# Kernel optimization log

Measured on AMD Instinct MI355X. Metric: run time of the kernel, lower is better.

## Reference

```python
import jax, jax.numpy as jnp
import numpy as np

N, E = 40000, 640000
IN_DIM, HID, HEADS, OUT, NC, ASSIGN = 128, 16, 8, 128, 2, 100
SIGMA = 0.5
F_HID = HID * HEADS  # 128 = hidden_dim * n_heads


def _edge_softmax(logits, dst, n):
    # softmax over incoming edges of each destination node (DGL edge_softmax)
    m = jax.ops.segment_max(logits, dst, num_segments=n)
    ex = jnp.exp(logits - m[dst])
    den = jax.ops.segment_sum(ex, dst, num_segments=n)
    return ex / den[dst]


def _gat_conv(h, src, dst, W, al, ar, b):
    # DGL GATConv: fc (no bias) -> per-head additive attention -> edge softmax -> scatter-sum
    nH, D = al.shape
    feat = (h @ W).reshape(h.shape[0], nH, D)            # [N,H,D]
    el = (feat * al).sum(-1)                              # [N,H]
    er = (feat * ar).sum(-1)                              # [N,H]
    logits = jax.nn.leaky_relu(el[src] + er[dst], 0.2)    # [E,H]
    a = _edge_softmax(logits, dst, h.shape[0])            # [E,H]
    out = jax.ops.segment_sum(feat[src] * a[..., None], dst, num_segments=h.shape[0])
    return out + b                                        # [N,H,D]


def _bn(x, g, b, eps=1e-5):
    mu = x.mean(0)
    v = x.var(0)
    return g * (x - mu) * jax.lax.rsqrt(v + eps) + b


def _gat_layer(h, src, dst, W, al, ar, b, g, bt):
    x = _gat_conv(h, src, dst, W, al, ar, b).reshape(h.shape[0], -1)
    x = jax.nn.elu(_bn(x, g, bt))
    return h + x  # residual: in_dim == out_dim*heads


def _mask(x):
    # h[torch.isinf(h)] = 1e9
    return jnp.where(jnp.isinf(x), 1e9, x)


def setup_inputs():
    key = jax.random.key(0)
    ks = jax.random.split(key, 20)
    rn = lambda k, s: jax.random.normal(k, s, jnp.float32) * 0.1
    return {
        "h": jax.random.normal(ks[0], (N, IN_DIM), jnp.float32),
        "e": jax.random.normal(ks[1], (E, 4), jnp.float32),
        "src": jax.random.randint(ks[2], (E,), 0, N, jnp.int32),
        "dst": jax.random.randint(ks[3], (E,), 0, N, jnp.int32),
        "W_emb": rn(ks[4], (IN_DIM, F_HID)), "b_emb": jnp.zeros((F_HID,), jnp.float32),
        "Wg": rn(ks[5], (3, F_HID, F_HID)),
        "alg": rn(ks[6], (3, HEADS, HID)), "arg": rn(ks[7], (3, HEADS, HID)),
        "bg": jnp.zeros((3, HEADS, HID), jnp.float32),
        "gam": jnp.ones((3, F_HID), jnp.float32), "bet": jnp.zeros((3, F_HID), jnp.float32),
        "W3": rn(ks[8], (F_HID, OUT)), "al3": rn(ks[9], (1, OUT)), "ar3": rn(ks[10], (1, OUT)),
        "b3": jnp.zeros((1, OUT), jnp.float32),
        "gam3": jnp.ones((OUT,), jnp.float32), "bet3": jnp.zeros((OUT,), jnp.float32),
        "Wa": rn(ks[11], (F_HID, ASSIGN)), "ba": jnp.zeros((ASSIGN,), jnp.float32),
        "Wm1": rn(ks[12], (2 * OUT, OUT)), "bm1": jnp.zeros((OUT,), jnp.float32),
        "Wm2": rn(ks[13], (OUT, OUT // 2)), "bm2": jnp.zeros((OUT // 2,), jnp.float32),
        "Wm3": rn(ks[14], (OUT // 2, NC)), "bm3": jnp.zeros((NC,), jnp.float32),
    }


def reference(h, e, src, dst, W_emb, b_emb, Wg, alg, arg, bg, gam, bet,
              W3, al3, ar3, b3, gam3, bet3, Wa, ba,
              Wm1, bm1, Wm2, bm2, Wm3, bm3):
    del e  # edge_feat=False: forward never consumes edge features
    h = h @ W_emb + b_emb  # embedding_h (dropout p=0 -> identity)
    # layer 0: GATLayer
    h = _mask(_gat_layer(h, src, dst, Wg[0], alg[0], arg[0], bg[0], gam[0], bet[0]))
    # layer 1: biGATLayer -> (h, s): GAT update + soft assignment s with sigma mixing over coarse pool
    h_in = h
    h_fine = _gat_layer(h, src, dst, Wg[1], alg[1], arg[1], bg[1], gam[1], bet[1])
    s = jax.nn.softmax(h_in @ Wa + ba, axis=-1)            # [N, ASSIGN]
    h_coarse = s.T @ h_fine                                # [ASSIGN, F_HID]
    h = _mask(SIGMA * h_fine + (1.0 - SIGMA) * (s @ h_coarse))
    # layer 2: GATLayer
    h = _mask(_gat_layer(h, src, dst, Wg[2], alg[2], arg[2], bg[2], gam[2], bet[2]))
    # layer 3: GATLayer, 1 head, out_dim
    h = _mask(_gat_layer(h, src, dst, W3, al3, ar3, b3, gam3, bet3))
    # apply_edges: gather src/dst node feats, concat, MLPReadout (256->128->64->NC), inf-mask
    z = jnp.concatenate([h[src], h[dst]], axis=1)          # [E, 2*OUT]
    z = jax.nn.relu(z @ Wm1 + bm1)
    z = jax.nn.relu(z @ Wm2 + bm2)
    z = _mask(z @ Wm3 + bm3)
    return z, s
```

## Files before the change

### kernel.cpp

```cpp
#include <hip/hip_runtime.h>
#include <hip/hip_bf16.h>
#include <math.h>

#define N_ 40000
#define E_ 640000
#define CB_ 400
#define CR_ 100
#define SB_ 256
#define SNB_ 157

typedef short bf16x8 __attribute__((ext_vector_type(8)));
typedef float floatx4 __attribute__((ext_vector_type(4)));

__device__ __forceinline__ short f2bf(float f) {
    __hip_bfloat16 h = __float2bfloat16(f);
    return *reinterpret_cast<short*>(&h);
}
__device__ __forceinline__ float bf2f(short u) {
    unsigned int x = ((unsigned int)(unsigned short)u) << 16;
    return __int_as_float(x);
}
__device__ __forceinline__ float rdlane(float v, int l) {
    return __int_as_float(__builtin_amdgcn_readlane(__float_as_int(v), l));
}
__device__ __forceinline__ float bflo(unsigned int u) { return __int_as_float(u << 16); }
__device__ __forceinline__ float bfhi(unsigned int u) { return __int_as_float(u & 0xffff0000u); }

__global__ void k_count(const int* __restrict__ dst, int* __restrict__ counts) {
    for (int e = blockIdx.x * blockDim.x + threadIdx.x; e < E_; e += gridDim.x * blockDim.x)
        atomicAdd(&counts[dst[e]], 1);
}

__global__ __launch_bounds__(256) void k_scanA(const int* __restrict__ counts,
                                               int* __restrict__ excl,
                                               int* __restrict__ bsum) {
    int t = threadIdx.x;
    int i = blockIdx.x * SB_ + t;
    int v = (i < N_) ? counts[i] : 0;
    int lane = t & 63, wv = t >> 6;
    int x = v;
#pragma unroll
    for (int off = 1; off < 64; off <<= 1) {
        int y = __shfl_up(x, off);
        if (lane >= off) x += y;
    }
    __shared__ int wsum[4];
    __shared__ int woff[4];
    if (lane == 63) wsum[wv] = x;
    __syncthreads();
    if (t == 0) {
        int a = 0;
#pragma unroll
        for (int j = 0; j < 4; j++) { int tv = wsum[j]; woff[j] = a; a += tv; }
        bsum[blockIdx.x] = a;
    }
    __syncthreads();
    if (i < N_) excl[i] = x - v + woff[wv];
}

__global__ __launch_bounds__(256) void k_scanB(int* __restrict__ bsum) {
    int t = threadIdx.x;
    int v = (t < SNB_) ? bsum[t] : 0;
    int lane = t & 63, wv = t >> 6;
    int x = v;
#pragma unroll
    for (int off = 1; off < 64; off <<= 1) {
        int y = __shfl_up(x, off);
        if (lane >= off) x += y;
    }
    __shared__ int wsum[4];
    __shared__ int woff[4];
    if (lane == 63) wsum[wv] = x;
    __syncthreads();
    if (t == 0) {
        int a = 0;
#pragma unroll
        for (int j = 0; j < 4; j++) { int tv = wsum[j]; woff[j] = a; a += tv; }
    }
    __syncthreads();
    if (t < SNB_) bsum[t] = x - v + woff[wv];
}

__global__ __launch_bounds__(256) void k_scanC(const int* __restrict__ excl,
                                               const int* __restrict__ bsum,
                                               int* __restrict__ rowptr,
                                               int* __restrict__ cursor) {
    int i = blockIdx.x * 256 + threadIdx.x;
    if (i < N_) {
        int r = excl[i] + bsum[i / SB_];
        rowptr[i] = r;
        cursor[i] = r;
    }
    if (i == N_) rowptr[N_] = E_;
}

__global__ void k_fill(const int* __restrict__ src, const int* __restrict__ dst,
                       int* __restrict__ cursor, int* __restrict__ srcv,
                       unsigned short* __restrict__ dstv, int* __restrict__ eidv) {
    for (int e = blockIdx.x * blockDim.x + threadIdx.x; e < E_; e += gridDim.x * blockDim.x) {
        int d = dst[e];
        int pos = atomicAdd(&cursor[d], 1);
        srcv[pos] = src[e];
        dstv[pos] = (unsigned short)d;
        eidv[pos] = e;
    }
}

__global__ __launch_bounds__(256) void k_prep_all(const float* __restrict__ Wg,
                                                  const float* __restrict__ W3,
                                                  const float* __restrict__ Wm1,
                                                  short* __restrict__ WbT6) {
    int i = blockIdx.x * 256 + threadIdx.x;
    if (i >= 6 * 16384) return;
    int m = i >> 14;
    int r = i & 16383;
    int n = r >> 7, k = r & 127;
    const float* srcp;
    switch (m) {
        case 0: srcp = Wg; break;
        case 1: srcp = Wg + 16384; break;
        case 2: srcp = Wg + 32768; break;
        case 3: srcp = W3; break;
        case 4: srcp = Wm1; break;
        default: srcp = Wm1 + 16384; break;
    }
    WbT6[m * 16384 + n * 128 + k] = f2bf(srcp[k * 128 + n]);
}

__global__ __launch_bounds__(256) void k_prep_hilo(const float* __restrict__ W_emb,
                                                   const float* __restrict__ Wa,
                                                   short* __restrict__ WembT_hi,
                                                   short* __restrict__ WembT_lo,
                                                   short* __restrict__ WaT_hi,
                                                   short* __restrict__ WaT_lo) {
    int i = blockIdx.x * 256 + threadIdx.x;
    if (i >= 2 * 16384) return;
    int m = i >> 14;
    int r = i & 16383;
    int n = r >> 7, k = r & 127;
    if (m == 0) {
        float w = W_emb[k * 128 + n];
        short h = f2bf(w);
        WembT_hi[n * 128 + k] = h;
        WembT_lo[n * 128 + k] = f2bf(w - bf2f(h));
    } else {
        float w = (n < 100) ? Wa[k * 100 + n] : 0.f;
        short h = f2bf(w);
        WaT_hi[n * 128 + k] = h;
        WaT_lo[n * 128 + k] = f2bf(w - bf2f(h));
    }
}

__global__ __launch_bounds__(256) void k_mfma_hilo(const float* __restrict__ A,
                                                   const short* __restrict__ BT_hi,
                                                   const short* __restrict__ BT_lo,
                                                   const float* __restrict__ bias,
                                                   float* __restrict__ C, int ncols) {
    __shared__ short sAh[64 * 136];
    __shared__ short sAl[64 * 136];
    __shared__ short sBh[128 * 136];
    int t = threadIdx.x;
    int r0 = blockIdx.x * 64;
    {
        int n = t >> 1;
        int k0 = (t & 1) * 64;
#pragma unroll
        for (int j = 0; j < 8; j++) {
            bf16x8 v = *(const bf16x8*)(BT_hi + n * 128 + k0 + 8 * j);
            *(bf16x8*)(sBh + n * 136 + k0 + 8 * j) = v;
        }
    }
    {
        int r = t >> 2;
        int k0 = (t & 3) * 32;
        const float* ar = A + (size_t)(r0 + r) * 128 + k0;
#pragma unroll
        for (int j = 0; j < 4; j++) {
            float4 f0 = *(const float4*)(ar + 8 * j);
            float4 f1 = *(const float4*)(ar + 8 * j + 4);
            float x[8] = {f0.x, f0.y, f0.z, f0.w, f1.x, f1.y, f1.z, f1.w};
            bf16x8 vh, vl;
#pragma unroll
            for (int q = 0; q < 8; q++) {
                short hh = f2bf(x[q]);
                vh[q] = hh;
                vl[q] = f2bf(x[q] - bf2f(hh));
            }
            *(bf16x8*)(sAh + r * 136 + k0 + 8 * j) = vh;
            *(bf16x8*)(sAl + r * 136 + k0 + 8 * j) = vl;
        }
    }
    __syncthreads();
    int lane = t & 63, wv = t >> 6;
    int lm = lane & 15, quad = lane >> 4;
    int m0 = wv * 16;
    bf16x8 aH[4], aL[4];
#pragma unroll
    for (int kt = 0; kt < 4; kt++) {
        aH[kt] = *(const bf16x8*)(sAh + (m0 + lm) * 136 + kt * 32 + quad * 8);
        aL[kt] = *(const bf16x8*)(sAl + (m0 + lm) * 136 + kt * 32 + quad * 8);
    }
#pragma unroll
    for (int nt = 0; nt < 8; nt++) {
        const short* blp = BT_lo + (nt * 16 + lm) * 128 + quad * 8;
        floatx4 acc = (floatx4){0.f, 0.f, 0.f, 0.f};
#pragma unroll
        for (int kt = 0; kt < 4; kt++) {
            bf16x8 bH = *(const bf16x8*)(sBh + (nt * 16 + lm) * 136 + kt * 32 + quad * 8);
            bf16x8 bL = *(const bf16x8*)(blp + kt * 32);
            acc = __builtin_amdgcn_mfma_f32_16x16x32_bf16(aH[kt], bH, acc, 0, 0, 0);
            acc = __builtin_amdgcn_mfma_f32_16x16x32_bf16(aL[kt], bH, acc, 0, 0, 0);
            acc = __builtin_amdgcn_mfma_f32_16x16x32_bf16(aH[kt], bL, acc, 0, 0, 0);
        }
        int col = nt * 16 + lm;
        if (col < ncols) {
            float bv = bias ? bias[col] : 0.f;
#pragma unroll
            for (int r = 0; r < 4; r++) {
                int row = r0 + m0 + quad * 4 + r;
                C[(size_t)row * ncols + col] = acc[r] + bv;
            }
        }
    }
}

__global__ __launch_bounds__(256) void k_gemm_mfma(const float* __restrict__ A,
                                                   const short* __restrict__ WbT,
                                                   const float* __restrict__ bias,
                                                   short* __restrict__ C) {
    __shared__ short sA[64 * 136];
    __shared__ short sB[128 * 136];
    int t = threadIdx.x;
    int r0 = blockIdx.x * 64;
    {
        int n = t >> 1;
        int k0 = (t & 1) * 64;
#pragma unroll
        for (int j = 0; j < 8; j++) {
            bf16x8 v = *(const bf16x8*)(WbT + n * 128 + k0 + 8 * j);
            *(bf16x8*)(sB + n * 136 + k0 + 8 * j) = v;
        }
    }
    {
        int r = t >> 2;
        int k0 = (t & 3) * 32;
        const float* ar = A + (size_t)(r0 + r) * 128 + k0;
#pragma unroll
        for (int j = 0; j < 4; j++) {
            float4 f0 = *(const float4*)(ar + 8 * j);
            float4 f1 = *(const float4*)(ar + 8 * j + 4);
            bf16x8 v;
            v[0] = f2bf(f0.x); v[1] = f2bf(f0.y); v[2] = f2bf(f0.z); v[3] = f2bf(f0.w);
            v[4] = f2bf(f1.x); v[5] = f2bf(f1.y); v[6] = f2bf(f1.z); v[7] = f2bf(f1.w);
            *(bf16x8*)(sA + r * 136 + k0 + 8 * j) = v;
        }
    }
    __syncthreads();
    int lane = t & 63, wv = t >> 6;
    int lm = lane & 15, quad = lane >> 4;
    int m0 = wv * 16;
    bf16x8 aF[4];
#pragma unroll
    for (int kt = 0; kt < 4; kt++)
        aF[kt] = *(const bf16x8*)(sA + (m0 + lm) * 136 + kt * 32 + quad * 8);
#pragma unroll
    for (int nt = 0; nt < 8; nt++) {
        floatx4 acc = (floatx4){0.f, 0.f, 0.f, 0.f};
#pragma unroll
        for (int kt = 0; kt < 4; kt++) {
            bf16x8 bF = *(const bf16x8*)(sB + (nt * 16 + lm) * 136 + kt * 32 + quad * 8);
            acc = __builtin_amdgcn_mfma_f32_16x16x32_bf16(aF[kt], bF, acc, 0, 0, 0);
        }
        int col = nt * 16 + lm;
        float bv = bias ? bias[col] : 0.f;
#pragma unroll
        for (int r = 0; r < 4; r++) {
            int row = r0 + m0 + quad * 4 + r;
            C[(size_t)row * 128 + col] = f2bf(acc[r] + bv);
        }
    }
}

__global__ __launch_bounds__(256) void k_smax100(const float* __restrict__ logits,
                                                 float* __restrict__ s) {
    int lane = threadIdx.x & 63;
    int n = blockIdx.x * 4 + (threadIdx.x >> 6);
    if (n >= N_) return;
    bool act = lane < 50;
    float2 v = make_float2(-INFINITY, -INFINITY);
    if (act) v = *(const float2*)(logits + (size_t)n * 100 + 2 * lane);
    float mx = fmaxf(v.x, v.y);
#pragma unroll
    for (int off = 1; off < 64; off <<= 1) mx = fmaxf(mx, __shfl_xor(mx, off));
    float e0 = act ? __expf(v.x - mx) : 0.f;
    float e1 = act ? __expf(v.y - mx) : 0.f;
    float sm = e0 + e1;
#pragma unroll
    for (int off = 1; off < 64; off <<= 1) sm += __shfl_xor(sm, off);
    float inv = 1.f / sm;
    if (act) *(float2*)(s + (size_t)n * 100 + 2 * lane) = make_float2(e0 * inv, e1 * inv);
}

template <int H>
__global__ __launch_bounds__(256) void k_elr(const short* __restrict__ feat,
                                             const float* __restrict__ al,
                                             const float* __restrict__ ar,
                                             float* __restrict__ el, float* __restrict__ er) {
    int lane = threadIdx.x & 63;
    int n = blockIdx.x * 4 + (threadIdx.x >> 6);
    if (n >= N_) return;
    unsigned int u = *(const unsigned int*)(feat + (size_t)n * 128 + 2 * lane);
    float fx = bflo(u), fy = bfhi(u);
    float2 a = *(const float2*)(al + 2 * lane);
    float2 b = *(const float2*)(ar + 2 * lane);
    float pl = fx * a.x + fy * a.y;
    float pr = fx * b.x + fy * b.y;
    constexpr int G = 64 / H;
#pragma unroll
    for (int off = 1; off < G; off <<= 1) {
        pl += __shfl_xor(pl, off);
        pr += __shfl_xor(pr, off);
    }
    if ((lane & (G - 1)) == 0) {
        int hh = lane / G;
        el[(size_t)n * H + hh] = pl;
        er[(size_t)n * H + hh] = pr;
    }
}

template <int H>
__global__ __launch_bounds__(256) void k_gat_agg(const short* __restrict__ feat,
                                                 const float* __restrict__ el,
                                                 const float* __restrict__ er,
                                                 const int* __restrict__ rowptr,
                                                 const int* __restrict__ srcv,
                                                 const float* __restrict__ bias,
                                                 float* __restrict__ xout) {
    int lane = threadIdx.x & 63;
    int gw = (blockIdx.x * blockDim.x + threadIdx.x) >> 6;
    int nw = (gridDim.x * blockDim.x) >> 6;
    constexpr int LH = (H == 8) ? 3 : 0;
    int h = lane & (H - 1);
    int f0 = 2 * lane;
    int hf = (H == 8) ? (lane >> 3) : 0;

    for (int n = gw; n < N_; n += nw) {
        int beg = rowptr[n], end = rowptr[n + 1];
        if (beg == end) {
            *(float2*)(xout + (size_t)n * 128 + f0) = *(const float2*)(bias + f0);
            continue;
        }
        float ern = er[(size_t)n * H + h];
        float m = -INFINITY, ss = 0.f;
        for (int e = beg + (lane >> LH); e < end; e += (64 >> LH)) {
            int sI = srcv[e];
            float x = el[(size_t)sI * H + h] + ern;
            float lr = x > 0.f ? x : 0.2f * x;
            if (lr > m) { ss = ss * __expf(m - lr) + 1.f; m = lr; }
            else ss += __expf(lr - m);
        }
#pragma unroll
        for (int off = H; off < 64; off <<= 1) {
            float om = __shfl_xor(m, off);
            float os = __shfl_xor(ss, off);
            float nm = fmaxf(m, om);
            float p1 = (m == -INFINITY) ? 0.f : ss * __expf(m - nm);
            float p2 = (om == -INFINITY) ? 0.f : os * __expf(om - nm);
            m = nm; ss = p1 + p2;
        }
        float inv_d = 1.f / ss;
        int endm1 = end - 1;
        float accx = 0.f, accy = 0.f;
        for (int e0 = beg; e0 < end; e0 += 16) {
            int le = lane >> 3;
            int eLA = e0 + le, eLB = e0 + 8 + le;
            int eCA = eLA <= endm1 ? eLA : endm1;
            int eCB = eLB <= endm1 ? eLB : endm1;
            int sLA = srcv[eCA];
            int sLB = srcv[eCB];
            float xA = el[(size_t)sLA * H + h] + ern;
            float xB = el[(size_t)sLB * H + h] + ern;
            float lrA = xA > 0.f ? xA : 0.2f * xA;
            float lrB = xB > 0.f ? xB : 0.2f * xB;
            float wA = __expf(lrA - m) * inv_d;
            float wB = __expf(lrB - m) * inv_d;
            if (eLA > endm1) wA = 0.f;
            if (eLB > endm1) wB = 0.f;
            bool haveB = (e0 + 8) < end;
            unsigned int uuA[8], uuB[8];
#pragma unroll
            for (int j = 0; j < 8; j++) {
                int sj = __builtin_amdgcn_readlane(sLA, j * 8);
                uuA[j] = *(const unsigned int*)(feat + (size_t)sj * 128 + f0);
            }
            if (haveB) {
#pragma unroll
                for (int j = 0; j < 8; j++) {
                    int sj = __builtin_amdgcn_readlane(sLB, j * 8);
                    uuB[j] = *(const unsigned int*)(feat + (size_t)sj * 128 + f0);
                }
            }
#pragma unroll
            for (int j = 0; j < 8; j++) {
                float aj;
                if (H == 8) aj = __shfl(wA, j * 8 + hf);
                else        aj = rdlane(wA, j * 8);
                accx += aj * bflo(uuA[j]);
                accy += aj * bfhi(uuA[j]);
            }
            if (haveB) {
#pragma unroll
                for (int j = 0; j < 8; j++) {
                    float aj;
                    if (H == 8) aj = __shfl(wB, j * 8 + hf);
                    else        aj = rdlane(wB, j * 8);
                    accx += aj * bflo(uuB[j]);
                    accy += aj * bfhi(uuB[j]);
                }
            }
        }
        float2 b2 = *(const float2*)(bias + f0);
        *(float2*)(xout + (size_t)n * 128 + f0) = make_float2(accx + b2.x, accy + b2.y);
    }
}

__global__ __launch_bounds__(256) void k_bn_stats(const float* __restrict__ x,
                                                  float* __restrict__ sum,
                                                  float* __restrict__ sumsq) {
    __shared__ float ls[256], lq[256];
    int t = threadIdx.x;
    int col = t & 127, half = t >> 7;
    float s = 0.f, q = 0.f;
    for (int r = blockIdx.x * 2 + half; r < N_; r += gridDim.x * 2) {
        float v = x[(size_t)r * 128 + col];
        s += v; q += v * v;
    }
    ls[t] = s; lq[t] = q;
    __syncthreads();
    if (t < 128) {
        atomicAdd(&sum[col], ls[t] + ls[t + 128]);
        atomicAdd(&sumsq[col], lq[t] + lq[t + 128]);
    }
}

__global__ __launch_bounds__(256) void k_bn_apply(const float* __restrict__ x,
                                                  const float* __restrict__ hprev,
                                                  const float* __restrict__ sum,
                                                  const float* __restrict__ sumsq,
                                                  const float* __restrict__ g,
                                                  const float* __restrict__ b,
                                                  float* __restrict__ out, int do_mask) {
    int i = blockIdx.x * blockDim.x + threadIdx.x;
    if (i >= N_ * 128) return;
    int c = i & 127;
    const float invN = 1.f / (float)N_;
    float mu = sum[c] * invN;
    float var = sumsq[c] * invN - mu * mu;
    float inv = rsqrtf(var + 1e-5f);
    float y = g[c] * (x[i] - mu) * inv + b[c];
    y = y > 0.f ? y : (__expf(y) - 1.f);
    float hv = hprev[i] + y;
    if (do_mask && isinf(hv)) hv = 1e9f;
    out[i] = hv;
}

__global__ __launch_bounds__(512) void k_coarse_part(const float* __restrict__ s,
                                                     const float* __restrict__ hf,
                                                     float* __restrict__ part) {
    int t = threadIdx.x;
    int c = t & 127;
    int g = t >> 7;
    int lane = t & 63;
    float acc[25];
#pragma unroll
    for (int a = 0; a < 25; a++) acc[a] = 0.f;
    int n0 = blockIdx.x * CR_;
    for (int n = n0; n < n0 + CR_; n += 2) {
        float hv0 = hf[(size_t)n * 128 + c];
        float hv1 = hf[(size_t)(n + 1) * 128 + c];
        float sv0 = 0.f, sv1 = 0.f;
        if (lane < 25) {
            sv0 = s[(size_t)n * 100 + 25 * g + lane];
            sv1 = s[(size_t)(n + 1) * 100 + 25 * g + lane];
        }
#pragma unroll
        for (int a = 0; a < 25; ++a) {
            float a0 = rdlane(sv0, a);
            float a1 = rdlane(sv1, a);
            acc[a] += a0 * hv0 + a1 * hv1;
        }
    }
    float* dstp = part + (size_t)blockIdx.x * 12800 + (size_t)(25 * g) * 128 + c;
#pragma unroll
    for (int a = 0; a < 25; a++) dstp[a * 128] = acc[a];
}

__global__ __launch_bounds__(256) void k_coarse_reduce(const float* __restrict__ part,
                                                       float* __restrict__ hc) {
    int i = blockIdx.x * blockDim.x + threadIdx.x;
    if (i >= 12800) return;
    float s0 = 0.f, s1 = 0.f, s2 = 0.f, s3 = 0.f;
    for (int b = 0; b < CB_; b += 4) {
        s0 += part[(size_t)(b + 0) * 12800 + i];
        s1 += part[(size_t)(b + 1) * 12800 + i];
        s2 += part[(size_t)(b + 2) * 12800 + i];
        s3 += part[(size_t)(b + 3) * 12800 + i];
    }
    hc[i] = (s0 + s1) + (s2 + s3);
}

__global__ __launch_bounds__(256) void k_combine(const float* __restrict__ s,
                                                 const float* __restrict__ hc,
                                                 const float* __restrict__ hfine,
                                                 float* __restrict__ hout) {
    __shared__ float ssh[16 * 100];
    int t = threadIdx.x;
    int n0 = blockIdx.x * 16;
    for (int u = t; u < 1600; u += 256) ssh[u] = s[(size_t)n0 * 100 + u];
    __syncthreads();
    int c = t & 127, g = t >> 7;
    float acc[8];
#pragma unroll
    for (int r = 0; r < 8; r++) acc[r] = 0.f;
    const float* hcp = hc + c;
    for (int a = 0; a < 100; a += 4) {
        float h0 = hcp[(a + 0) * 128];
        float h1 = hcp[(a + 1) * 128];
        float h2 = hcp[(a + 2) * 128];
        float h3 = hcp[(a + 3) * 128];
#pragma unroll
        for (int r = 0; r < 8; r++) {
            float4 sv = *(const float4*)(ssh + (g * 8 + r) * 100 + a);
            acc[r] += sv.x * h0 + sv.y * h1 + sv.z * h2 + sv.w * h3;
        }
    }
#pragma unroll
    for (int r = 0; r < 8; r++) {
        int row = n0 + g * 8 + r;
        float v = 0.5f * hfine[(size_t)row * 128 + c] + 0.5f * acc[r];
        if (isinf(v)) v = 1e9f;
        hout[(size_t)row * 128 + c] = v;
    }
}

__global__ __launch_bounds__(256) void k_prep_w(const float* __restrict__ Wm2,
                                                short* __restrict__ Wm2T) {
    int i = blockIdx.x * blockDim.x + threadIdx.x;
    if (i >= 64 * 128) return;
    int n = i & 63, k = i >> 6;
    Wm2T[n * 128 + k] = f2bf(Wm2[k * 64 + n]);
}

__global__ __launch_bounds__(256) void k_edge_mlp3(const short* __restrict__ Pb,
                                                   const short* __restrict__ Qb,
                                                   const int* __restrict__ srcv,
                                                   const unsigned short* __restrict__ dstv,
                                                   const int* __restrict__ eidv,
                                                   const short* __restrict__ Wm2T,
                                                   const float* __restrict__ bm2,
                                                   const float* __restrict__ Wm3,
                                                   const float* __restrict__ bm3,
                                                   float* __restrict__ zout) {
    __shared__ short sW[64 * 128];
    int t = threadIdx.x;
    for (int u = t; u < 1024; u += 256) {
        int n = u >> 4, k16 = u & 15;
        int phys = (n << 4) | (k16 ^ (n & 15));
        *(bf16x8*)(sW + phys * 8) = *(const bf16x8*)(Wm2T + n * 128 + k16 * 8);
    }
    int lane = t & 63;
    int lm = lane & 15, quad = lane >> 4;
    float bv[4], w30[4], w31[4];
#pragma unroll
    for (int nt = 0; nt < 4; nt++) {
        int n = nt * 16 + lm;
        bv[nt] = bm2[n]; w30[nt] = Wm3[2 * n]; w31[nt] = Wm3[2 * n + 1];
    }
    float b30 = bm3[0], b31 = bm3[1];
    __syncthreads();

    int gw = (blockIdx.x * blockDim.x + t) >> 6;
    int nw = (gridDim.x * blockDim.x) >> 6;

    for (int tile = gw; tile < E_ / 16; tile += nw) {
        int p0 = tile * 16;
        int sI = srcv[p0 + lm];
        int dI = (int)dstv[p0 + lm];
        const short* pr = Pb + (size_t)sI * 128 + quad * 8;
        const short* qr = Qb + (size_t)dI * 128 + quad * 8;
        uint4 pu[4], qu[4];
#pragma unroll
        for (int kt = 0; kt < 4; kt++) {
            pu[kt] = *(const uint4*)(pr + kt * 32);
            qu[kt] = *(const uint4*)(qr + kt * 32);
        }
        bf16x8 aF[4];
#pragma unroll
        for (int kt = 0; kt < 4; kt++) {
            unsigned int pv[4] = {pu[kt].x, pu[kt].y, pu[kt].z, pu[kt].w};
            unsigned int qv[4] = {qu[kt].x, qu[kt].y, qu[kt].z, qu[kt].w};
            union { uint4 u; bf16x8 v; } cv;
            unsigned int rr[4];
#pragma unroll
            for (int j = 0; j < 4; j++) {
                float fl = fmaxf(bflo(pv[j]) + bflo(qv[j]), 0.f);
                float fh = fmaxf(bfhi(pv[j]) + bfhi(qv[j]), 0.f);
                rr[j] = (unsigned int)(unsigned short)f2bf(fl) |
                        ((unsigned int)(unsigned short)f2bf(fh) << 16);
            }
            cv.u.x = rr[0]; cv.u.y = rr[1]; cv.u.z = rr[2]; cv.u.w = rr[3];
            aF[kt] = cv.v;
        }
        float pz0[4] = {0.f, 0.f, 0.f, 0.f};
        float pz1[4] = {0.f, 0.f, 0.f, 0.f};
#pragma unroll
        for (int nt = 0; nt < 4; nt++) {
            floatx4 acc = (floatx4){0.f, 0.f, 0.f, 0.f};
#pragma unroll
            for (int kt = 0; kt < 4; kt++) {
                int phys = ((nt * 16 + lm) << 4) | (((kt << 2) | quad) ^ lm);
                bf16x8 bF = *(const bf16x8*)(sW + phys * 8);
                acc = __builtin_amdgcn_mfma_f32_16x16x32_bf16(aF[kt], bF, acc, 0, 0, 0);
            }
#pragma unroll
            for (int r = 0; r < 4; r++) {
                float u = fmaxf(acc[r] + bv[nt], 0.f);
                pz0[r] += u * w30[nt];
                pz1[r] += u * w31[nt];
            }
        }
#pragma unroll
        for (int off = 1; off < 16; off <<= 1) {
#pragma unroll
            for (int r = 0; r < 4; r++) {
                pz0[r] += __shfl_xor(pz0[r], off);
                pz1[r] += __shfl_xor(pz1[r], off);
            }
        }
        if (lm < 4) {
            int eid = eidv[p0 + quad * 4 + lm];
            float z0 = pz0[lm] + b30;
            float z1 = pz1[lm] + b31;
            if (isinf(z0)) z0 = 1e9f;
            if (isinf(z1)) z1 = 1e9f;
            *(float2*)(zout + (size_t)eid * 2) = make_float2(z0, z1);
        }
    }
}

extern "C" void kernel_launch(void* const* d_in, const int* in_sizes, int n_in,
                              void* d_out, int out_size, void* d_ws, size_t ws_size,
                              hipStream_t stream) {
    const float* h_in  = (const float*)d_in[0];
    const int*   src   = (const int*)d_in[2];
    const int*   dst   = (const int*)d_in[3];
    const float* W_emb = (const float*)d_in[4];
    const float* b_emb = (const float*)d_in[5];
    const float* Wg    = (const float*)d_in[6];
    const float* alg   = (const float*)d_in[7];
    const float* arg_  = (const float*)d_in[8];
    const float* bg    = (const float*)d_in[9];
    const float* gam   = (const float*)d_in[10];
    const float* bet   = (const float*)d_in[11];
    const float* W3    = (const float*)d_in[12];
    const float* al3   = (const float*)d_in[13];
    const float* ar3   = (const float*)d_in[14];
    const float* b3    = (const float*)d_in[15];
    const float* gam3  = (const float*)d_in[16];
    const float* bet3  = (const float*)d_in[17];
    const float* Wa    = (const float*)d_in[18];
    const float* ba    = (const float*)d_in[19];
    const float* Wm1   = (const float*)d_in[20];
    const float* bm1   = (const float*)d_in[21];
    const float* Wm2   = (const float*)d_in[22];
    const float* bm2   = (const float*)d_in[23];
    const float* Wm3   = (const float*)d_in[24];
    const float* bm3   = (const float*)d_in[25];

    float* zout = (float*)d_out;
    float* sout = zout + (size_t)E_ * 2;

    float* ws = (float*)d_ws;
    size_t o = 0;
    float* h_cur = ws + o; o += (size_t)N_ * 128;
    float* xbuf  = ws + o; o += (size_t)N_ * 128;
    float* featb = ws + o; o += (size_t)N_ * 128;
    float* el    = ws + o; o += (size_t)N_ * 8;
    float* er    = ws + o; o += (size_t)N_ * 8;
    float* colsum = ws + o; o += 128;
    float* colsq  = ws + o; o += 128;
    float* hc     = ws + o; o += 100 * 128;
    short* Wm2T = (short*)(ws + o); o += (64 * 128) / 2;
    short* WbT6 = (short*)(ws + o); o += (6 * 16384) / 2;
    short* WembT_hi = (short*)(ws + o); o += 16384 / 2;
    short* WembT_lo = (short*)(ws + o); o += 16384 / 2;
    short* WaT_hi   = (short*)(ws + o); o += 16384 / 2;
    short* WaT_lo   = (short*)(ws + o); o += 16384 / 2;
    int* counts = (int*)(ws + o); o += N_;
    int* rowptr = (int*)(ws + o); o += N_ + 4;
    int* cursor = (int*)(ws + o); o += N_;
    int* srcv   = (int*)(ws + o); o += E_;
    unsigned short* dstv = (unsigned short*)(ws + o); o += E_ / 2;
    int* eidv   = (int*)(ws + o); o += E_;
    int* bsum   = (int*)(ws + o); o += SNB_ + 4;

    short* featw = (short*)featb;

    hipMemsetAsync(counts, 0, N_ * sizeof(int), stream);
    k_count<<<1024, 256, 0, stream>>>(dst, counts);
    k_scanA<<<SNB_, 256, 0, stream>>>(counts, eidv, bsum);
    k_scanB<<<1, 256, 0, stream>>>(bsum);
    k_scanC<<<SNB_ + 1, 256, 0, stream>>>(eidv, bsum, rowptr, cursor);
    k_fill<<<1024, 256, 0, stream>>>(src, dst, cursor, srcv, dstv, eidv);
    k_prep_w<<<32, 256, 0, stream>>>(Wm2, Wm2T);
    k_prep_all<<<384, 256, 0, stream>>>(Wg, W3, Wm1, WbT6);
    k_prep_hilo<<<128, 256, 0, stream>>>(W_emb, Wa, WembT_hi, WembT_lo, WaT_hi, WaT_lo);

    k_mfma_hilo<<<N_ / 64, 256, 0, stream>>>(h_in, WembT_hi, WembT_lo, b_emb, h_cur, 128);

    k_gemm_mfma<<<N_ / 64, 256, 0, stream>>>(h_cur, WbT6 + 0 * 16384, nullptr, featw);
    k_elr<8><<<N_ / 4, 256, 0, stream>>>(featw, alg + 0 * 128, arg_ + 0 * 128, el, er);
    k_gat_agg<8><<<2048, 256, 0, stream>>>(featw, el, er, rowptr, srcv, bg + 0 * 128, xbuf);
    hipMemsetAsync(colsum, 0, 256 * sizeof(float), stream);
    k_bn_stats<<<512, 256, 0, stream>>>(xbuf, colsum, colsq);
    k_bn_apply<<<(N_ * 128) / 256, 256, 0, stream>>>(xbuf, h_cur, colsum, colsq,
                                                     gam + 0 * 128, bet + 0 * 128, h_cur, 1);

    k_mfma_hilo<<<N_ / 64, 256, 0, stream>>>(h_cur, WaT_hi, WaT_lo, ba, xbuf, 100);
    k_smax100<<<N_ / 4, 256, 0, stream>>>(xbuf, sout);
    k_gemm_mfma<<<N_ / 64, 256, 0, stream>>>(h_cur, WbT6 + 1 * 16384, nullptr, featw);
    k_elr<8><<<N_ / 4, 256, 0, stream>>>(featw, alg + 1 * 128, arg_ + 1 * 128, el, er);
    k_gat_agg<8><<<2048, 256, 0, stream>>>(featw, el, er, rowptr, srcv, bg + 1 * 128, xbuf);
    hipMemsetAsync(colsum, 0, 256 * sizeof(float), stream);
    k_bn_stats<<<512, 256, 0, stream>>>(xbuf, colsum, colsq);
    k_bn_apply<<<(N_ * 128) / 256, 256, 0, stream>>>(xbuf, h_cur, colsum, colsq,
                                                     gam + 1 * 128, bet + 1 * 128, xbuf, 0);
    k_coarse_part<<<CB_, 512, 0, stream>>>(sout, xbuf, featb);
    k_coarse_reduce<<<50, 256, 0, stream>>>(featb, hc);
    k_combine<<<N_ / 16, 256, 0, stream>>>(sout, hc, xbuf, h_cur);

    k_gemm_mfma<<<N_ / 64, 256, 0, stream>>>(h_cur, WbT6 + 2 * 16384, nullptr, featw);
    k_elr<8><<<N_ / 4, 256, 0, stream>>>(featw, alg + 2 * 128, arg_ + 2 * 128, el, er);
    k_gat_agg<8><<<2048, 256, 0, stream>>>(featw, el, er, rowptr, srcv, bg + 2 * 128, xbuf);
    hipMemsetAsync(colsum, 0, 256 * sizeof(float), stream);
    k_bn_stats<<<512, 256, 0, stream>>>(xbuf, colsum, colsq);
    k_bn_apply<<<(N_ * 128) / 256, 256, 0, stream>>>(xbuf, h_cur, colsum, colsq,
                                                     gam + 2 * 128, bet + 2 * 128, h_cur, 1);

    k_gemm_mfma<<<N_ / 64, 256, 0, stream>>>(h_cur, WbT6 + 3 * 16384, nullptr, featw);
    k_elr<1><<<N_ / 4, 256, 0, stream>>>(featw, al3, ar3, el, er);
    k_gat_agg<1><<<2048, 256, 0, stream>>>(featw, el, er, rowptr, srcv, b3, xbuf);
    hipMemsetAsync(colsum, 0, 256 * sizeof(float), stream);
    k_bn_stats<<<512, 256, 0, stream>>>(xbuf, colsum, colsq);
    k_bn_apply<<<(N_ * 128) / 256, 256, 0, stream>>>(xbuf, h_cur, colsum, colsq,
                                                     gam3, bet3, h_cur, 1);

    short* Pb = (short*)featb;
    short* Qb = Pb + (size_t)N_ * 128;
    k_gemm_mfma<<<N_ / 64, 256, 0, stream>>>(h_cur, WbT6 + 4 * 16384, bm1, Pb);
    k_gemm_mfma<<<N_ / 64, 256, 0, stream>>>(h_cur, WbT6 + 5 * 16384, nullptr, Qb);
    k_edge_mlp3<<<2048, 256, 0, stream>>>(Pb, Qb, srcv, dstv, eidv, Wm2T, bm2, Wm3, bm3, zout);
}
```

Baseline: 824.7 us.

## Fuse batchnorm statistics into GAT aggregation and unroll softmax max pass

Removes the separate k_bn_stats kernel by accumulating per-column sum and sum-of-squares inside k_gat_agg as each output row is written. Each block reduces its partials in shared memory and issues atomics, so the 20 MB re-read of xbuf and one launch per layer go away. The edge-softmax first pass is also unrolled by two so two gathers are in flight at once. The cost is extra registers, shared memory and per-block atomics in the aggregation kernel, which may lower occupancy.

```diff
diff --git a/kernel.cpp b/kernel.cpp
--- a/kernel.cpp
+++ b/kernel.cpp
@@ -335,29 +335,51 @@
                                                  const int* __restrict__ rowptr,
                                                  const int* __restrict__ srcv,
                                                  const float* __restrict__ bias,
-                                                 float* __restrict__ xout) {
-    int lane = threadIdx.x & 63;
-    int gw = (blockIdx.x * blockDim.x + threadIdx.x) >> 6;
+                                                 float* __restrict__ xout,
+                                                 float* __restrict__ csum,
+                                                 float* __restrict__ csq) {
+    int t = threadIdx.x;
+    int lane = t & 63;
+    int gw = (blockIdx.x * blockDim.x + t) >> 6;
     int nw = (gridDim.x * blockDim.x) >> 6;
     constexpr int LH = (H == 8) ? 3 : 0;
+    constexpr int STEP = 64 >> LH;
     int h = lane & (H - 1);
     int f0 = 2 * lane;
     int hf = (H == 8) ? (lane >> 3) : 0;
 
+    float stx = 0.f, sty = 0.f, qtx = 0.f, qty = 0.f;
+
     for (int n = gw; n < N_; n += nw) {
         int beg = rowptr[n], end = rowptr[n + 1];
         if (beg == end) {
-            *(float2*)(xout + (size_t)n * 128 + f0) = *(const float2*)(bias + f0);
+            float2 b2 = *(const float2*)(bias + f0);
+            *(float2*)(xout + (size_t)n * 128 + f0) = b2;
+            stx += b2.x; sty += b2.y;
+            qtx += b2.x * b2.x; qty += b2.y * b2.y;
             continue;
         }
         float ern = er[(size_t)n * H + h];
         float m = -INFINITY, ss = 0.f;
-        for (int e = beg + (lane >> LH); e < end; e += (64 >> LH)) {
-            int sI = srcv[e];
-            float x = el[(size_t)sI * H + h] + ern;
-            float lr = x > 0.f ? x : 0.2f * x;
-            if (lr > m) { ss = ss * __expf(m - lr) + 1.f; m = lr; }
-            else ss += __expf(lr - m);
+        int e = beg + (lane >> LH);
+        for (; e + STEP < end; e += 2 * STEP) {
+            int sA = srcv[e];
+            int sB = srcv[e + STEP];
+            float xA = el[(size_t)sA * H + h] + ern;
+            float xB = el[(size_t)sB * H + h] + ern;
+            float lrA = xA > 0.f ? xA : 0.2f * xA;
+            float lrB = xB > 0.f ? xB : 0.2f * xB;
+            if (lrA > m) { ss = ss * __expf(m - lrA) + 1.f; m = lrA; }
+            else ss += __expf(lrA - m);
+            if (lrB > m) { ss = ss * __expf(m - lrB) + 1.f; m = lrB; }
+            else ss += __expf(lrB - m);
+        }
+        if (e < end) {
+            int sA = srcv[e];
+            float xA = el[(size_t)sA * H + h] + ern;
+            float lrA = xA > 0.f ? xA : 0.2f * xA;
+            if (lrA > m) { ss = ss * __expf(m - lrA) + 1.f; m = lrA; }
+            else ss += __expf(lrA - m);
         }
 #pragma unroll
         for (int off = H; off < 64; off <<= 1) {
@@ -420,26 +442,24 @@
             }
         }
         float2 b2 = *(const float2*)(bias + f0);
-        *(float2*)(xout + (size_t)n * 128 + f0) = make_float2(accx + b2.x, accy + b2.y);
-    }
-}
-
-__global__ __launch_bounds__(256) void k_bn_stats(const float* __restrict__ x,
-                                                  float* __restrict__ sum,
-                                                  float* __restrict__ sumsq) {
-    __shared__ float ls[256], lq[256];
-    int t = threadIdx.x;
-    int col = t & 127, half = t >> 7;
-    float s = 0.f, q = 0.f;
-    for (int r = blockIdx.x * 2 + half; r < N_; r += gridDim.x * 2) {
-        float v = x[(size_t)r * 128 + col];
-        s += v; q += v * v;
-    }
-    ls[t] = s; lq[t] = q;
-    __syncthreads();
-    if (t < 128) {
-        atomicAdd(&sum[col], ls[t] + ls[t + 128]);
-        atomicAdd(&sumsq[col], lq[t] + lq[t + 128]);
+        float ox = accx + b2.x, oy = accy + b2.y;
+        *(float2*)(xout + (size_t)n * 128 + f0) = make_float2(ox, oy);
+        stx += ox; sty += oy;
+        qtx += ox * ox; qty += oy * oy;
+    }
+
+    __shared__ float red[4][256];
+    red[0][t] = stx; red[1][t] = sty; red[2][t] = qtx; red[3][t] = qty;
+    __syncthreads();
+    if (t < 64) {
+        float a0 = red[0][t] + red[0][t + 64] + red[0][t + 128] + red[0][t + 192];
+        float a1 = red[1][t] + red[1][t + 64] + red[1][t + 128] + red[1][t + 192];
+        float q0 = red[2][t] + red[2][t + 64] + red[2][t + 128] + red[2][t + 192];
+        float q1 = red[3][t] + red[3][t + 64] + red[3][t + 128] + red[3][t + 192];
+        atomicAdd(&csum[2 * t], a0);
+        atomicAdd(&csum[2 * t + 1], a1);
+        atomicAdd(&csq[2 * t], q0);
+        atomicAdd(&csq[2 * t + 1], q1);
     }
 }
 
@@ -720,9 +740,9 @@
 
     k_gemm_mfma<<<N_ / 64, 256, 0, stream>>>(h_cur, WbT6 + 0 * 16384, nullptr, featw);
     k_elr<8><<<N_ / 4, 256, 0, stream>>>(featw, alg + 0 * 128, arg_ + 0 * 128, el, er);
-    k_gat_agg<8><<<2048, 256, 0, stream>>>(featw, el, er, rowptr, srcv, bg + 0 * 128, xbuf);
     hipMemsetAsync(colsum, 0, 256 * sizeof(float), stream);
-    k_bn_stats<<<512, 256, 0, stream>>>(xbuf, colsum, colsq);
+    k_gat_agg<8><<<2048, 256, 0, stream>>>(featw, el, er, rowptr, srcv, bg + 0 * 128, xbuf,
+                                           colsum, colsq);
     k_bn_apply<<<(N_ * 128) / 256, 256, 0, stream>>>(xbuf, h_cur, colsum, colsq,
                                                      gam + 0 * 128, bet + 0 * 128, h_cur, 1);
 
@@ -730,9 +750,9 @@
     k_smax100<<<N_ / 4, 256, 0, stream>>>(xbuf, sout);
     k_gemm_mfma<<<N_ / 64, 256, 0, stream>>>(h_cur, WbT6 + 1 * 16384, nullptr, featw);
     k_elr<8><<<N_ / 4, 256, 0, stream>>>(featw, alg + 1 * 128, arg_ + 1 * 128, el, er);
-    k_gat_agg<8><<<2048, 256, 0, stream>>>(featw, el, er, rowptr, srcv, bg + 1 * 128, xbuf);
     hipMemsetAsync(colsum, 0, 256 * sizeof(float), stream);
-    k_bn_stats<<<512, 256, 0, stream>>>(xbuf, colsum, colsq);
+    k_gat_agg<8><<<2048, 256, 0, stream>>>(featw, el, er, rowptr, srcv, bg + 1 * 128, xbuf,
+                                           colsum, colsq);
     k_bn_apply<<<(N_ * 128) / 256, 256, 0, stream>>>(xbuf, h_cur, colsum, colsq,
                                                      gam + 1 * 128, bet + 1 * 128, xbuf, 0);
     k_coarse_part<<<CB_, 512, 0, stream>>>(sout, xbuf, featb);
@@ -741,17 +761,17 @@
 
     k_gemm_mfma<<<N_ / 64, 256, 0, stream>>>(h_cur, WbT6 + 2 * 16384, nullptr, featw);
     k_elr<8><<<N_ / 4, 256, 0, stream>>>(featw, alg + 2 * 128, arg_ + 2 * 128, el, er);
-    k_gat_agg<8><<<2048, 256, 0, stream>>>(featw, el, er, rowptr, srcv, bg + 2 * 128, xbuf);
     hipMemsetAsync(colsum, 0, 256 * sizeof(float), stream);
-    k_bn_stats<<<512, 256, 0, stream>>>(xbuf, colsum, colsq);
+    k_gat_agg<8><<<2048, 256, 0, stream>>>(featw, el, er, rowptr, srcv, bg + 2 * 128, xbuf,
+                                           colsum, colsq);
     k_bn_apply<<<(N_ * 128) / 256, 256, 0, stream>>>(xbuf, h_cur, colsum, colsq,
                                                      gam + 2 * 128, bet + 2 * 128, h_cur, 1);
 
     k_gemm_mfma<<<N_ / 64, 256, 0, stream>>>(h_cur, WbT6 + 3 * 16384, nullptr, featw);
     k_elr<1><<<N_ / 4, 256, 0, stream>>>(featw, al3, ar3, el, er);
-    k_gat_agg<1><<<2048, 256, 0, stream>>>(featw, el, er, rowptr, srcv, b3, xbuf);
     hipMemsetAsync(colsum, 0, 256 * sizeof(float), stream);
-    k_bn_stats<<<512, 256, 0, stream>>>(xbuf, colsum, colsq);
+    k_gat_agg<1><<<2048, 256, 0, stream>>>(featw, el, er, rowptr, srcv, b3, xbuf,
+                                           colsum, colsq);
     k_bn_apply<<<(N_ * 128) / 256, 256, 0, stream>>>(xbuf, h_cur, colsum, colsq,
                                                      gam3, bet3, h_cur, 1);
 
```

After: 1.067 ms. +29.3%, slower.
